# Kernel optimization log

Measured on AMD Instinct MI355X. Metric: run time of the kernel, lower is better.

The kernel has to match this reference:

```python
import jax, jax.numpy as jnp
import numpy as np

B, TE, TD, H = 8, 512, 128, 256

def setup_inputs() -> dict:
    key = jax.random.key(0)
    k1, k2, k3, k4, k5 = jax.random.split(key, 5)
    return {
        "encoder_outputs": jax.random.normal(k1, (B, TE, H), dtype=jnp.float32),
        "decoder_outputs": jax.random.normal(k2, (B, TD, H), dtype=jnp.float32),
        "W_a": jax.random.normal(k3, (H, H), dtype=jnp.float32) * (1.0 / np.sqrt(H)),
        "U_a": jax.random.normal(k4, (H, H), dtype=jnp.float32) * (1.0 / np.sqrt(H)),
        "V_a": jax.random.normal(k5, (H, 1), dtype=jnp.float32) * (1.0 / np.sqrt(H)),
    }

def reference(encoder_outputs, decoder_outputs, W_a, U_a, V_a):
    # Bahdanau additive attention.
    enc_proj = jnp.einsum("beh,hk->bek", encoder_outputs, W_a)   # [B,TE,H]
    dec_proj = jnp.einsum("bdh,hk->bdk", decoder_outputs, U_a)   # [B,TD,H]
    # Broadcast add -> tanh -> project with V_a: [B,TD,TE]
    score = jnp.tanh(enc_proj[:, None, :, :] + dec_proj[:, :, None, :])  # [B,TD,TE,H]
    score = jnp.einsum("bdeh,h->bde", score, V_a[:, 0])          # [B,TD,TE]
    attention_weights = jax.nn.softmax(score, axis=-1)           # over encoder positions
    context = jnp.einsum("bde,beh->bdh", attention_weights, encoder_outputs)
    return (context, attention_weights)
```

## Files before the change

kernel.cpp:

```cpp
#include <hip/hip_runtime.h>
#include <hip/hip_bf16.h>

#ifndef __has_builtin
#define __has_builtin(x) 0
#endif

constexpr int B_ = 8, TE_ = 512, TD_ = 128, H_ = 256;
constexpr float TWO_LOG2E = 2.8853900817779268f;
constexpr float LOG2E = 1.4426950408889634f;

typedef float  vf2    __attribute__((ext_vector_type(2)));
typedef short  bf16x8 __attribute__((ext_vector_type(8)));
typedef float  f32x4  __attribute__((ext_vector_type(4)));

__device__ __forceinline__ float exp2_fast(float x) {
#if __has_builtin(__builtin_amdgcn_exp2f)
  return __builtin_amdgcn_exp2f(x);
#else
  return exp2f(x);
#endif
}
__device__ __forceinline__ float rcp_fast(float x) {
#if __has_builtin(__builtin_amdgcn_rcpf)
  return __builtin_amdgcn_rcpf(x);
#else
  return 1.0f / x;
#endif
}
__device__ __forceinline__ vf2 fma2(vf2 a, vf2 b, vf2 c) {
#if __has_builtin(__builtin_elementwise_fma)
  return __builtin_elementwise_fma(a, b, c);
#else
  vf2 r; r.x = __fmaf_rn(a.x, b.x, c.x); r.y = __fmaf_rn(a.y, b.y, c.y); return r;
#endif
}
__device__ __forceinline__ void bf16split(float x, unsigned short& hi, unsigned short& lo) {
  unsigned u = __float_as_uint(x);
  hi = (unsigned short)(u >> 16);
  float hif = __uint_as_float((unsigned)hi << 16);
  lo = (unsigned short)(__float_as_uint(x - hif) >> 16);
}

__global__ __launch_bounds__(256)
void proj_mfma(const float* __restrict__ enc, const float* __restrict__ dec,
               const float* __restrict__ W, const float* __restrict__ U,
               float* __restrict__ ep, float* __restrict__ dp) {
  __shared__ unsigned short Ah[32][40], Al[32][40], Bh[32][40], Bl[32][40];
  const int tid = threadIdx.x;
  const int mt = blockIdx.x;
  const int n0 = blockIdx.y * 32;
  const float* A; const float* Bm; float* C; int row0;
  if (mt < 128) { A = enc; Bm = W; C = ep; row0 = mt * 32; }
  else          { A = dec; Bm = U; C = dp; row0 = (mt - 128) * 32; }
  const int w = tid >> 6, lane = tid & 63;
  const int mw = (w & 1) * 16, nw = (w >> 1) * 16;
  const int quad = lane >> 4, l16 = lane & 15;
  const int am = tid >> 3, ak = (tid & 7) * 4;
  const int bn = tid & 31, bk = (tid >> 5) * 4;

  f32x4 acc = {0.f, 0.f, 0.f, 0.f};
  for (int k0 = 0; k0 < H_; k0 += 32) {
    float4 a4 = *(const float4*)&A[(long)(row0 + am) * H_ + k0 + ak];
    unsigned short h0, l0, h1, l1, h2, l2, h3, l3;
    bf16split(a4.x, h0, l0); bf16split(a4.y, h1, l1);
    bf16split(a4.z, h2, l2); bf16split(a4.w, h3, l3);
    *(ushort4*)&Ah[am][ak] = make_ushort4(h0, h1, h2, h3);
    *(ushort4*)&Al[am][ak] = make_ushort4(l0, l1, l2, l3);
    float b0 = Bm[(long)(k0 + bk + 0) * H_ + n0 + bn];
    float b1 = Bm[(long)(k0 + bk + 1) * H_ + n0 + bn];
    float b2 = Bm[(long)(k0 + bk + 2) * H_ + n0 + bn];
    float b3 = Bm[(long)(k0 + bk + 3) * H_ + n0 + bn];
    bf16split(b0, h0, l0); bf16split(b1, h1, l1);
    bf16split(b2, h2, l2); bf16split(b3, h3, l3);
    *(ushort4*)&Bh[bn][bk] = make_ushort4(h0, h1, h2, h3);
    *(ushort4*)&Bl[bn][bk] = make_ushort4(l0, l1, l2, l3);
    __syncthreads();
    bf16x8 ah = *(const bf16x8*)&Ah[mw + l16][quad * 8];
    bf16x8 al = *(const bf16x8*)&Al[mw + l16][quad * 8];
    bf16x8 bh = *(const bf16x8*)&Bh[nw + l16][quad * 8];
    bf16x8 bl = *(const bf16x8*)&Bl[nw + l16][quad * 8];
    acc = __builtin_amdgcn_mfma_f32_16x16x32_bf16(ah, bh, acc, 0, 0, 0);
    acc = __builtin_amdgcn_mfma_f32_16x16x32_bf16(ah, bl, acc, 0, 0, 0);
    acc = __builtin_amdgcn_mfma_f32_16x16x32_bf16(al, bh, acc, 0, 0, 0);
    __syncthreads();
  }
#pragma unroll
  for (int r = 0; r < 4; ++r)
    C[(long)(row0 + mw + quad * 4 + r) * H_ + n0 + nw + l16] =
        exp2_fast(acc[r] * TWO_LOG2E);
}

__global__ __launch_bounds__(256)
void score_kernel(const float* __restrict__ ep, const float* __restrict__ dp,
                  const float* __restrict__ v, float* __restrict__ sc) {
  __shared__ __align__(16) float eps[32][68];
  __shared__ __align__(16) float dps[16][68];
  __shared__ __align__(16) float vs[64];
  const int tid = threadIdx.x;
  const int bz = blockIdx.z;
  const int b = bz >> 1;
  const int h_lo = (bz & 1) * 128;
  const int e0 = blockIdx.x * 32;
  const int d0 = blockIdx.y * 16;
  const int e = tid & 31;
  const int dg = tid >> 5;
  vf2 acc0 = {0.f, 0.f}, acc1 = {0.f, 0.f};

  for (int h0 = h_lo; h0 < h_lo + 128; h0 += 64) {
#pragma unroll
    for (int i = 0; i < 2; ++i) {
      int idx = tid + i * 256;
      int r = idx >> 4, c = (idx & 15) << 2;
      *(float4*)&eps[r][c] = *(const float4*)&ep[(long)(b * TE_ + e0 + r) * H_ + h0 + c];
    }
    {
      int r = tid >> 4, c = (tid & 15) << 2;
      *(float4*)&dps[r][c] = *(const float4*)&dp[(long)(b * TD_ + d0 + r) * H_ + h0 + c];
    }
    if (tid < 16) {
      float4 v4 = *(const float4*)&v[h0 + tid * 4];
      float4 o; o.x = -2.f * v4.x; o.y = -2.f * v4.y; o.z = -2.f * v4.z; o.w = -2.f * v4.w;
      *(float4*)&vs[tid * 4] = o;
    }
    __syncthreads();
    const vf2 one2 = {1.f, 1.f};
#pragma unroll
    for (int hh = 0; hh < 64; hh += 4) {
      float4 evf = *(const float4*)&eps[e][hh];
      float4 vvf = *(const float4*)&vs[hh];
      float4 daf = *(const float4*)&dps[dg * 2 + 0][hh];
      float4 dbf = *(const float4*)&dps[dg * 2 + 1][hh];
      vf2 ev0 = {evf.x, evf.y}, ev1 = {evf.z, evf.w};
      vf2 vv0 = {vvf.x, vvf.y}, vv1 = {vvf.z, vvf.w};
      vf2 da0 = {daf.x, daf.y}, da1 = {daf.z, daf.w};
      vf2 db0 = {dbf.x, dbf.y}, db1 = {dbf.z, dbf.w};
      vf2 t0 = ev0 * da0 + one2;
      vf2 t1 = ev1 * da1 + one2;
      vf2 u0 = ev0 * db0 + one2;
      vf2 u1 = ev1 * db1 + one2;
      vf2 r0, r1, s0, s1;
      r0.x = rcp_fast(t0.x); r0.y = rcp_fast(t0.y);
      r1.x = rcp_fast(t1.x); r1.y = rcp_fast(t1.y);
      s0.x = rcp_fast(u0.x); s0.y = rcp_fast(u0.y);
      s1.x = rcp_fast(u1.x); s1.y = rcp_fast(u1.y);
      acc0 = fma2(vv0, r0, acc0); acc0 = fma2(vv1, r1, acc0);
      acc1 = fma2(vv0, s0, acc1); acc1 = fma2(vv1, s1, acc1);
    }
    __syncthreads();
  }
  long base = ((long)(bz & 1) * B_ * TD_ + (long)b * TD_ + d0 + dg * 2) * TE_ + e0 + e;
  sc[base] = acc0.x + acc0.y;
  sc[base + TE_] = acc1.x + acc1.y;
}

__global__ __launch_bounds__(64)
void softmax_kernel(const float* __restrict__ sc, float* __restrict__ attn) {
  const long row = blockIdx.x;
  const float* p0 = sc + row * TE_;
  const float* p1 = sc + ((long)B_ * TD_ + row) * TE_;
  float* pout = attn + row * TE_;
  const int t = threadIdx.x;
  float x[8];
  float m = -1e30f;
#pragma unroll
  for (int k = 0; k < 8; ++k) {
    x[k] = p0[t + 64 * k] + p1[t + 64 * k];
    m = fmaxf(m, x[k]);
  }
#pragma unroll
  for (int off = 32; off; off >>= 1) m = fmaxf(m, __shfl_xor(m, off, 64));
  float s = 0.f;
#pragma unroll
  for (int k = 0; k < 8; ++k) { x[k] = exp2_fast((x[k] - m) * LOG2E); s += x[k]; }
#pragma unroll
  for (int off = 32; off; off >>= 1) s += __shfl_xor(s, off, 64);
  const float r = rcp_fast(s);
#pragma unroll
  for (int k = 0; k < 8; ++k) pout[t + 64 * k] = x[k] * r;
}

__global__ __launch_bounds__(256)
void ctx_mfma(const float* __restrict__ attn, const float* __restrict__ enc,
              float* __restrict__ ctx) {
  __shared__ unsigned short Ah[32][40], Al[32][40], Bh[32][40], Bl[32][40];
  const int tid = threadIdx.x;
  const int m0 = blockIdx.x * 32;
  const int n0 = blockIdx.y * 32;
  const int b = blockIdx.z;
  const float* A = attn + (long)b * TD_ * TE_;
  const float* E = enc + (long)b * TE_ * H_;
  const int w = tid >> 6, lane = tid & 63;
  const int mw = (w & 1) * 16, nw = (w >> 1) * 16;
  const int quad = lane >> 4, l16 = lane & 15;
  const int am = tid >> 3, ak = (tid & 7) * 4;
  const int bn = tid & 31, bk = (tid >> 5) * 4;

  f32x4 acc = {0.f, 0.f, 0.f, 0.f};
  for (int k0 = 0; k0 < TE_; k0 += 32) {
    float4 a4 = *(const float4*)&A[(long)(m0 + am) * TE_ + k0 + ak];
    unsigned short h0, l0, h1, l1, h2, l2, h3, l3;
    bf16split(a4.x, h0, l0); bf16split(a4.y, h1, l1);
    bf16split(a4.z, h2, l2); bf16split(a4.w, h3, l3);
    *(ushort4*)&Ah[am][ak] = make_ushort4(h0, h1, h2, h3);
    *(ushort4*)&Al[am][ak] = make_ushort4(l0, l1, l2, l3);
    float b0 = E[(long)(k0 + bk + 0) * H_ + n0 + bn];
    float b1 = E[(long)(k0 + bk + 1) * H_ + n0 + bn];
    float b2 = E[(long)(k0 + bk + 2) * H_ + n0 + bn];
    float b3 = E[(long)(k0 + bk + 3) * H_ + n0 + bn];
    bf16split(b0, h0, l0); bf16split(b1, h1, l1);
    bf16split(b2, h2, l2); bf16split(b3, h3, l3);
    *(ushort4*)&Bh[bn][bk] = make_ushort4(h0, h1, h2, h3);
    *(ushort4*)&Bl[bn][bk] = make_ushort4(l0, l1, l2, l3);
    __syncthreads();
    bf16x8 ah = *(const bf16x8*)&Ah[mw + l16][quad * 8];
    bf16x8 al = *(const bf16x8*)&Al[mw + l16][quad * 8];
    bf16x8 bh = *(const bf16x8*)&Bh[nw + l16][quad * 8];
    bf16x8 bl = *(const bf16x8*)&Bl[nw + l16][quad * 8];
    acc = __builtin_amdgcn_mfma_f32_16x16x32_bf16(ah, bh, acc, 0, 0, 0);
    acc = __builtin_amdgcn_mfma_f32_16x16x32_bf16(ah, bl, acc, 0, 0, 0);
    acc = __builtin_amdgcn_mfma_f32_16x16x32_bf16(al, bh, acc, 0, 0, 0);
    __syncthreads();
  }
#pragma unroll
  for (int r = 0; r < 4; ++r)
    ctx[((long)b * TD_ + m0 + mw + quad * 4 + r) * H_ + n0 + nw + l16] = acc[r];
}

extern "C" void kernel_launch(void* const* d_in, const int* in_sizes, int n_in,
                              void* d_out, int out_size, void* d_ws, size_t ws_size,
                              hipStream_t stream) {
  const float* enc = (const float*)d_in[0];
  const float* dec = (const float*)d_in[1];
  const float* Wa  = (const float*)d_in[2];
  const float* Ua  = (const float*)d_in[3];
  const float* Va  = (const float*)d_in[4];

  float* out  = (float*)d_out;
  float* ctx  = out;
  float* attn = out + (long)B_ * TD_ * H_;

  float* ep = (float*)d_ws;
  float* dp = ep + (long)B_ * TE_ * H_;
  float* sc = dp + (long)B_ * TD_ * H_;

  proj_mfma<<<dim3(160, 8), 256, 0, stream>>>(enc, dec, Wa, Ua, ep, dp);
  score_kernel<<<dim3(TE_ / 32, TD_ / 16, 2 * B_), 256, 0, stream>>>(ep, dp, Va, sc);
  softmax_kernel<<<dim3(B_ * TD_), 64, 0, stream>>>(sc, attn);
  ctx_mfma<<<dim3(TD_ / 32, H_ / 32, B_), 256, 0, stream>>>(attn, enc, ctx);
}
```

Baseline: 99.38 us.

## Fuse softmax into score and context kernels using unnormalized exp and atomic row sums

Removes the separate softmax kernel: the score kernel now covers all of H per block, exponentiates scores without max subtraction, writes unnormalized values and atomically accumulates per-row sums. The context kernel scales rows by the reciprocal sum, writes attention weights, and uses them in the MFMA product. This saves a launch and a pass over the score buffer, but halves the score grid and relies on scores being bounded so exp cannot overflow.

After: 105.1 us. 5.7% more time.

```diff
diff --git a/kernel.cpp b/kernel.cpp
--- a/kernel.cpp
+++ b/kernel.cpp
@@ -44,9 +44,14 @@
 __global__ __launch_bounds__(256)
 void proj_mfma(const float* __restrict__ enc, const float* __restrict__ dec,
                const float* __restrict__ W, const float* __restrict__ U,
-               float* __restrict__ ep, float* __restrict__ dp) {
+               float* __restrict__ ep, float* __restrict__ dp,
+               float* __restrict__ rowsum) {
   __shared__ unsigned short Ah[32][40], Al[32][40], Bh[32][40], Bl[32][40];
   const int tid = threadIdx.x;
+  if (blockIdx.x == 0 && blockIdx.y == 0) {
+    float4 z = {0.f, 0.f, 0.f, 0.f};
+    *(float4*)&rowsum[tid * 4] = z;
+  }
   const int mt = blockIdx.x;
   const int n0 = blockIdx.y * 32;
   const float* A; const float* Bm; float* C; int row0;
@@ -92,21 +97,20 @@
 
 __global__ __launch_bounds__(256)
 void score_kernel(const float* __restrict__ ep, const float* __restrict__ dp,
-                  const float* __restrict__ v, float* __restrict__ sc) {
+                  const float* __restrict__ v, float* __restrict__ u,
+                  float* __restrict__ rowsum) {
   __shared__ __align__(16) float eps[32][68];
   __shared__ __align__(16) float dps[16][68];
   __shared__ __align__(16) float vs[64];
   const int tid = threadIdx.x;
-  const int bz = blockIdx.z;
-  const int b = bz >> 1;
-  const int h_lo = (bz & 1) * 128;
+  const int b = blockIdx.z;
   const int e0 = blockIdx.x * 32;
   const int d0 = blockIdx.y * 16;
   const int e = tid & 31;
   const int dg = tid >> 5;
   vf2 acc0 = {0.f, 0.f}, acc1 = {0.f, 0.f};
 
-  for (int h0 = h_lo; h0 < h_lo + 128; h0 += 64) {
+  for (int h0 = 0; h0 < H_; h0 += 64) {
 #pragma unroll
     for (int i = 0; i < 2; ++i) {
       int idx = tid + i * 256;
@@ -148,59 +152,53 @@
     }
     __syncthreads();
   }
-  long base = ((long)(bz & 1) * B_ * TD_ + (long)b * TD_ + d0 + dg * 2) * TE_ + e0 + e;
-  sc[base] = acc0.x + acc0.y;
-  sc[base + TE_] = acc1.x + acc1.y;
-}
-
-__global__ __launch_bounds__(64)
-void softmax_kernel(const float* __restrict__ sc, float* __restrict__ attn) {
-  const long row = blockIdx.x;
-  const float* p0 = sc + row * TE_;
-  const float* p1 = sc + ((long)B_ * TD_ + row) * TE_;
-  float* pout = attn + row * TE_;
-  const int t = threadIdx.x;
-  float x[8];
-  float m = -1e30f;
-#pragma unroll
-  for (int k = 0; k < 8; ++k) {
-    x[k] = p0[t + 64 * k] + p1[t + 64 * k];
-    m = fmaxf(m, x[k]);
-  }
-#pragma unroll
-  for (int off = 32; off; off >>= 1) m = fmaxf(m, __shfl_xor(m, off, 64));
-  float s = 0.f;
-#pragma unroll
-  for (int k = 0; k < 8; ++k) { x[k] = exp2_fast((x[k] - m) * LOG2E); s += x[k]; }
-#pragma unroll
-  for (int off = 32; off; off >>= 1) s += __shfl_xor(s, off, 64);
-  const float r = rcp_fast(s);
-#pragma unroll
-  for (int k = 0; k < 8; ++k) pout[t + 64 * k] = x[k] * r;
+  const float uv0 = exp2_fast((acc0.x + acc0.y) * LOG2E);
+  const float uv1 = exp2_fast((acc1.x + acc1.y) * LOG2E);
+  long base = ((long)b * TD_ + d0 + dg * 2) * TE_ + e0 + e;
+  u[base] = uv0;
+  u[base + TE_] = uv1;
+  float s0 = uv0, s1 = uv1;
+#pragma unroll
+  for (int off = 16; off; off >>= 1) {
+    s0 += __shfl_xor(s0, off, 64);
+    s1 += __shfl_xor(s1, off, 64);
+  }
+  if (e == 0) {
+    const int row = b * TD_ + d0 + dg * 2;
+    atomicAdd(&rowsum[row], s0);
+    atomicAdd(&rowsum[row + 1], s1);
+  }
 }
 
 __global__ __launch_bounds__(256)
-void ctx_mfma(const float* __restrict__ attn, const float* __restrict__ enc,
+void ctx_mfma(const float* __restrict__ u, const float* __restrict__ rowsum,
+              const float* __restrict__ enc, float* __restrict__ attn,
               float* __restrict__ ctx) {
   __shared__ unsigned short Ah[32][40], Al[32][40], Bh[32][40], Bl[32][40];
   const int tid = threadIdx.x;
   const int m0 = blockIdx.x * 32;
   const int n0 = blockIdx.y * 32;
   const int b = blockIdx.z;
-  const float* A = attn + (long)b * TD_ * TE_;
+  const float* A = u + ((long)b * TD_ + m0) * TE_;
   const float* E = enc + (long)b * TE_ * H_;
   const int w = tid >> 6, lane = tid & 63;
   const int mw = (w & 1) * 16, nw = (w >> 1) * 16;
   const int quad = lane >> 4, l16 = lane & 15;
   const int am = tid >> 3, ak = (tid & 7) * 4;
   const int bn = tid & 31, bk = (tid >> 5) * 4;
+  const float rinv = rcp_fast(rowsum[b * TD_ + m0 + am]);
+  const bool writeAttn = (n0 == 0);
+  float* arow = attn + ((long)b * TD_ + m0 + am) * TE_;
 
   f32x4 acc = {0.f, 0.f, 0.f, 0.f};
   for (int k0 = 0; k0 < TE_; k0 += 32) {
-    float4 a4 = *(const float4*)&A[(long)(m0 + am) * TE_ + k0 + ak];
+    float4 a4 = *(const float4*)&A[(long)am * TE_ + k0 + ak];
+    float4 p;
+    p.x = a4.x * rinv; p.y = a4.y * rinv; p.z = a4.z * rinv; p.w = a4.w * rinv;
+    if (writeAttn) *(float4*)&arow[k0 + ak] = p;
     unsigned short h0, l0, h1, l1, h2, l2, h3, l3;
-    bf16split(a4.x, h0, l0); bf16split(a4.y, h1, l1);
-    bf16split(a4.z, h2, l2); bf16split(a4.w, h3, l3);
+    bf16split(p.x, h0, l0); bf16split(p.y, h1, l1);
+    bf16split(p.z, h2, l2); bf16split(p.w, h3, l3);
     *(ushort4*)&Ah[am][ak] = make_ushort4(h0, h1, h2, h3);
     *(ushort4*)&Al[am][ak] = make_ushort4(l0, l1, l2, l3);
     float b0 = E[(long)(k0 + bk + 0) * H_ + n0 + bn];
@@ -241,10 +239,10 @@
 
   float* ep = (float*)d_ws;
   float* dp = ep + (long)B_ * TE_ * H_;
-  float* sc = dp + (long)B_ * TD_ * H_;
-
-  proj_mfma<<<dim3(160, 8), 256, 0, stream>>>(enc, dec, Wa, Ua, ep, dp);
-  score_kernel<<<dim3(TE_ / 32, TD_ / 16, 2 * B_), 256, 0, stream>>>(ep, dp, Va, sc);
-  softmax_kernel<<<dim3(B_ * TD_), 64, 0, stream>>>(sc, attn);
-  ctx_mfma<<<dim3(TD_ / 32, H_ / 32, B_), 256, 0, stream>>>(attn, enc, ctx);
-}
+  float* u  = dp + (long)B_ * TD_ * H_;
+  float* rowsum = u + (long)B_ * TD_ * TE_;
+
+  proj_mfma<<<dim3(160, 8), 256, 0, stream>>>(enc, dec, Wa, Ua, ep, dp, rowsum);
+  score_kernel<<<dim3(TE_ / 32, TD_ / 16, B_), 256, 0, stream>>>(ep, dp, Va, u, rowsum);
+  ctx_mfma<<<dim3(TD_ / 32, H_ / 32, B_), 256, 0, stream>>>(u, rowsum, enc, attn, ctx);
+}
```
